# Optimization experiments

Measured on AMD Instinct MI355X. Metric: run time of the kernel, lower is better.

Reference implementation:

```python
import jax, jax.numpy as jnp
import numpy as np

B, S, V = 2, 336, 8      # batch, seq_len, n_vars
D, H, P = 256, 8, 96     # d_model, num_heads, pred_len
DK = D // H
OUT_CHN = 8
EPS = 1e-5


def _layernorm(x, g, b):
    mu = jnp.mean(x, axis=-1, keepdims=True)
    var = jnp.var(x, axis=-1, keepdims=True)
    return (x - mu) * jax.lax.rsqrt(var + EPS) * g + b


def _attn_ff(src, Wq, bq, Wk, bk, Wv, bv, Wo, bo, ln1_g, ln1_b):
    # src: [N, L, D]; manual MHA + residual + layernorm (dropout=0)
    N, L, _ = src.shape
    q = (src @ Wq + bq).reshape(N, L, H, DK).transpose(0, 2, 1, 3)
    k = (src @ Wk + bk).reshape(N, L, H, DK).transpose(0, 2, 1, 3)
    v = (src @ Wv + bv).reshape(N, L, H, DK).transpose(0, 2, 1, 3)
    scores = jnp.einsum('nhqd,nhkd->nhqk', q, k) / np.sqrt(DK).astype(np.float32)
    attn = jax.nn.softmax(scores, axis=-1)
    o = jnp.einsum('nhqk,nhkd->nhqd', attn, v)
    o = o.transpose(0, 2, 1, 3).reshape(N, L, D) @ Wo + bo
    return _layernorm(src + o, ln1_g, ln1_b)


def setup_inputs() -> dict:
    key = jax.random.key(0)
    ks = jax.random.split(key, 8)
    s = 1.0 / np.sqrt(D)
    return {
        'x': jax.random.normal(ks[0], (B, S, V), dtype=jnp.float32),
        'emb_w': jax.random.normal(ks[1], (1, D), dtype=jnp.float32),
        'emb_b': jnp.zeros((D,), jnp.float32),
        'Wq': jax.random.normal(ks[2], (D, D), dtype=jnp.float32) * s,
        'bq': jnp.zeros((D,), jnp.float32),
        'Wk': jax.random.normal(ks[3], (D, D), dtype=jnp.float32) * s,
        'bk': jnp.zeros((D,), jnp.float32),
        'Wv': jax.random.normal(ks[4], (D, D), dtype=jnp.float32) * s,
        'bv': jnp.zeros((D,), jnp.float32),
        'Wo': jax.random.normal(ks[5], (D, D), dtype=jnp.float32) * s,
        'bo': jnp.zeros((D,), jnp.float32),
        'ln1_g': jnp.ones((D,), jnp.float32),
        'ln1_b': jnp.zeros((D,), jnp.float32),
        'norm_g': jnp.ones((D,), jnp.float32),
        'norm_b': jnp.zeros((D,), jnp.float32),
        'proj_w': jax.random.normal(ks[6], (S * D, P), dtype=jnp.float32) / np.sqrt(S * D).astype(np.float32),
        'proj_b': jnp.zeros((P,), jnp.float32),
    }


def reference(x, emb_w, emb_b, Wq, bq, Wk, bk, Wv, bv, Wo, bo,
              ln1_g, ln1_b, norm_g, norm_b, proj_w, proj_b):
    attn_p = (Wq, bq, Wk, bk, Wv, bv, Wo, bo, ln1_g, ln1_b)
    # x: [B,S,V] -> [B,V,S] -> embed each scalar to D
    e = x.transpose(0, 2, 1)[..., None] @ emb_w + emb_b  # [B,V,S,D]
    for _ in range(10):
        # attention over time axis (shared weights)
        e = _attn_ff(e.reshape(B * V, S, D), *attn_p).reshape(B, V, S, D)
        e = _layernorm(e.transpose(0, 2, 1, 3), norm_g, norm_b)  # [B,S,V,D]
        # attention over variable axis (same weights)
        e = _attn_ff(e.reshape(B * S, V, D), *attn_p).reshape(B, S, V, D)
        e = e.transpose(0, 2, 1, 3)  # [B,V,S,D]
    out = e.reshape(B, V, S * D) @ proj_w + proj_b  # [B,V,P]
    return out.transpose(0, 2, 1)[:, :, :OUT_CHN]  # [B,P,out_chn]
```

## Files before the change

### kernel.cpp

```cpp
#include <hip/hip_runtime.h>

#define SS 336
#define VV 8
#define DD 256
#define DKK 32
#define NTOK 5376
#define NTD (NTOK * DD)
#define ATT_SCALE 0.17677669529663687f
#define LN_EPS 1e-5f

typedef _Float16 f16x8 __attribute__((ext_vector_type(8)));
typedef _Float16 f16x4v __attribute__((ext_vector_type(4)));
typedef __attribute__((ext_vector_type(4))) float f32x4;

__device__ inline _Float16 f2h(float f) { return (_Float16)f; }

__global__ __launch_bounds__(256) void k_prep_w(
    const float* __restrict__ Wq, const float* __restrict__ Wk,
    const float* __restrict__ Wv, const float* __restrict__ Wo,
    _Float16* __restrict__ WT2) {
  int z = blockIdx.y;
  const float* W = (z == 0) ? Wq : (z == 1) ? Wk : (z == 2) ? Wv : Wo;
  int o = blockIdx.x * 256 + threadIdx.x;
  int blk = o >> 9;
  int idx = o & 511;
  int lane = idx >> 3, j = idx & 7;
  int nt = blk >> 3, kb = blk & 7;
  int lcol = lane & 15, quad = lane >> 4;
  int n = nt * 16 + lcol;
  int k = kb * 32 + quad * 8 + j;
  WT2[(size_t)z * 65536 + o] = f2h(W[k * 256 + n]);
}

__global__ __launch_bounds__(256) void k_embed(
    const float* __restrict__ x, const float* __restrict__ ew,
    const float* __restrict__ eb, float* __restrict__ E,
    _Float16* __restrict__ E16) {
  int token = blockIdx.x;
  int n = token / SS, s = token - n * SS;
  int b = n >> 3, v = n & 7;
  float xv = x[(b * SS + s) * VV + v];
  int d = threadIdx.x;
  float val = fmaf(xv, ew[d], eb[d]);
  E[token * DD + d] = val;
  E16[token * DD + d] = f2h(val);
}

__global__ __launch_bounds__(256) void k_gemm_qkv(
    const _Float16* __restrict__ A16, const _Float16* __restrict__ WT2,
    const float* __restrict__ c0, const float* __restrict__ c1,
    const float* __restrict__ c2,
    _Float16* __restrict__ H0, _Float16* __restrict__ H1,
    _Float16* __restrict__ H2) {
  int z = blockIdx.z;
  const float* bias = (z == 0) ? c0 : (z == 1) ? c1 : c2;
  _Float16* H       = (z == 0) ? H0 : (z == 1) ? H1 : H2;
  int m0 = blockIdx.x * 64;
  int tid = threadIdx.x;
  int wave = tid >> 6, lane = tid & 63;
  int wm = wave >> 1, wn = wave & 1;
  int quad = lane >> 4, lcol = lane & 15;
  int ntb = blockIdx.y * 8 + wn * 4;

  __shared__ _Float16 As[64 * 264];

  for (int c = tid; c < 2048; c += 256) {
    int row = c >> 5, seg = c & 31;
    *(f16x8*)&As[row * 264 + seg * 8] =
        *(const f16x8*)&A16[(size_t)(m0 + row) * 256 + seg * 8];
  }
  __syncthreads();

  f32x4 acc[2][4] = {};

  for (int kb = 0; kb < 8; ++kb) {
    int k0 = kb * 32;
    f16x8 af[2];
#pragma unroll
    for (int mt = 0; mt < 2; ++mt)
      af[mt] = *(const f16x8*)&As[(wm * 32 + mt * 16 + lcol) * 264 + k0 + quad * 8];
#pragma unroll
    for (int nt = 0; nt < 4; ++nt) {
      f16x8 bfr = *(const f16x8*)&WT2[(size_t)z * 65536 +
                                      ((ntb + nt) * 8 + kb) * 512 + lane * 8];
#pragma unroll
      for (int mt = 0; mt < 2; ++mt)
        acc[mt][nt] = __builtin_amdgcn_mfma_f32_16x16x32_f16(
            af[mt], bfr, acc[mt][nt], 0, 0, 0);
    }
  }

  float bsv[4];
#pragma unroll
  for (int nt = 0; nt < 4; ++nt) bsv[nt] = bias[(ntb + nt) * 16 + lcol];
#pragma unroll
  for (int mt = 0; mt < 2; ++mt) {
#pragma unroll
    for (int i = 0; i < 4; ++i) {
      int r = m0 + wm * 32 + mt * 16 + quad * 4 + i;
#pragma unroll
      for (int nt = 0; nt < 4; ++nt) {
        int c = (ntb + nt) * 16 + lcol;
        H[(size_t)r * 256 + c] = f2h(acc[mt][nt][i] + bsv[nt]);
      }
    }
  }
}

#define KSTR 36
#define VTSTR 344
#define PSTR 72
__global__ __launch_bounds__(512) void k_attn_time(
    const _Float16* __restrict__ Q, const _Float16* __restrict__ K,
    const _Float16* __restrict__ V, _Float16* __restrict__ O16) {
  int qg = blockIdx.x, h = blockIdx.y, n = blockIdx.z;
  int tid = threadIdx.x;
  int wave = tid >> 6, lane = tid & 63;
  int quad = lane >> 4, lcol = lane & 15;

  __shared__ _Float16 Ks[336 * KSTR];
  __shared__ _Float16 Vt[32 * VTSTR + 16];
  __shared__ _Float16 Ps[8][16 * PSTR];

  const size_t base = (size_t)(n * SS) * DD + h * DKK;

  for (int c = tid; c < 1344; c += 512) {
    int row = c >> 2, part = c & 3;
    f16x8 kv = *(const f16x8*)&K[base + (size_t)row * DD + part * 8];
    f16x4v klo = __builtin_shufflevector(kv, kv, 0, 1, 2, 3);
    f16x4v khi = __builtin_shufflevector(kv, kv, 4, 5, 6, 7);
    *(f16x4v*)&Ks[row * KSTR + part * 8] = klo;
    *(f16x4v*)&Ks[row * KSTR + part * 8 + 4] = khi;
    f16x8 vv = *(const f16x8*)&V[base + (size_t)row * DD + part * 8];
#pragma unroll
    for (int j = 0; j < 8; ++j) Vt[(part * 8 + j) * VTSTR + row] = vv[j];
  }
  for (int c = tid; c < 272; c += 512) {
    if (c < 256) {
      int d = c >> 3, col = 336 + (c & 7);
      Vt[d * VTSTR + col] = (_Float16)0.f;
    } else {
      Vt[32 * VTSTR + (c - 256)] = (_Float16)0.f;
    }
  }
  __syncthreads();

  _Float16* P = Ps[wave];
  const f16x8 onesv = {(_Float16)1.f, (_Float16)1.f, (_Float16)1.f, (_Float16)1.f,
                       (_Float16)1.f, (_Float16)1.f, (_Float16)1.f, (_Float16)1.f};
  const f32x4 z4 = {0.f, 0.f, 0.f, 0.f};

  int qt0 = qg ? 11 : 0;
  int qtend = qg ? 21 : 11;
  for (int qtile = qt0 + wave; qtile < qtend; qtile += 8) {
    int qb = qtile * 16;

    f16x8 qf = *(const f16x8*)&Q[base + (size_t)(qb + lcol) * DD + quad * 8];
    f32x4 accA = {0.f, 0.f, 0.f, 0.f};
    f32x4 accB = {0.f, 0.f, 0.f, 0.f};
    f32x4 lacc = {0.f, 0.f, 0.f, 0.f};
    float m_[4] = {-1e30f, -1e30f, -1e30f, -1e30f};

    for (int T = 0; T < 6; ++T) {
      int k0 = T * 64;
      bool full = (T < 5);
      f32x4 s[4];
      {
        const _Float16* kp = &Ks[(k0 + lcol) * KSTR + quad * 8];
        f16x4v a0 = *(const f16x4v*)kp;
        f16x4v b0 = *(const f16x4v*)(kp + 4);
        f16x8 kf = __builtin_shufflevector(a0, b0, 0, 1, 2, 3, 4, 5, 6, 7);
        s[0] = __builtin_amdgcn_mfma_f32_16x16x32_f16(qf, kf, z4, 0, 0, 0);
      }
      if (full) {
#pragma unroll
        for (int u = 1; u < 4; ++u) {
          const _Float16* kp = &Ks[(k0 + u * 16 + lcol) * KSTR + quad * 8];
          f16x4v a0 = *(const f16x4v*)kp;
          f16x4v b0 = *(const f16x4v*)(kp + 4);
          f16x8 kf = __builtin_shufflevector(a0, b0, 0, 1, 2, 3, 4, 5, 6, 7);
          s[u] = __builtin_amdgcn_mfma_f32_16x16x32_f16(qf, kf, z4, 0, 0, 0);
        }
      } else {
        s[1] = z4; s[2] = z4; s[3] = z4;
      }
      float sc[4][4], p[4][4], corr[4];
#pragma unroll
      for (int u = 0; u < 4; ++u)
#pragma unroll
        for (int i = 0; i < 4; ++i)
          sc[u][i] = (u == 0 || full) ? s[u][i] * ATT_SCALE : -1e30f;
#pragma unroll
      for (int i = 0; i < 4; ++i) {
        float t2 = fmaxf(fmaxf(sc[0][i], sc[1][i]), fmaxf(sc[2][i], sc[3][i]));
        t2 = fmaxf(t2, __shfl_xor(t2, 1));
        t2 = fmaxf(t2, __shfl_xor(t2, 2));
        t2 = fmaxf(t2, __shfl_xor(t2, 4));
        t2 = fmaxf(t2, __shfl_xor(t2, 8));
        float nm = fmaxf(m_[i], t2);
        corr[i] = __expf(m_[i] - nm);
        m_[i] = nm;
#pragma unroll
        for (int u = 0; u < 4; ++u) p[u][i] = __expf(sc[u][i] - nm);
        accA[i] *= corr[i];
        accB[i] *= corr[i];
        lacc[i] *= corr[i];
      }
#pragma unroll
      for (int i = 0; i < 4; ++i)
#pragma unroll
        for (int u = 0; u < 4; ++u)
          P[(quad * 4 + i) * PSTR + u * 16 + lcol] = f2h(p[u][i]);
      f16x8 pf0 = *(const f16x8*)&P[lcol * PSTR + quad * 8];
      lacc = __builtin_amdgcn_mfma_f32_16x16x32_f16(pf0, onesv, lacc, 0, 0, 0);
      f16x8 va0 = *(const f16x8*)&Vt[lcol * VTSTR + k0 + quad * 8];
      f16x8 vb0 = *(const f16x8*)&Vt[(16 + lcol) * VTSTR + k0 + quad * 8];
      accA = __builtin_amdgcn_mfma_f32_16x16x32_f16(pf0, va0, accA, 0, 0, 0);
      accB = __builtin_amdgcn_mfma_f32_16x16x32_f16(pf0, vb0, accB, 0, 0, 0);
      if (full) {
        f16x8 pf1 = *(const f16x8*)&P[lcol * PSTR + 32 + quad * 8];
        lacc = __builtin_amdgcn_mfma_f32_16x16x32_f16(pf1, onesv, lacc, 0, 0, 0);
        f16x8 va1 = *(const f16x8*)&Vt[lcol * VTSTR + k0 + 32 + quad * 8];
        f16x8 vb1 = *(const f16x8*)&Vt[(16 + lcol) * VTSTR + k0 + 32 + quad * 8];
        accA = __builtin_amdgcn_mfma_f32_16x16x32_f16(pf1, va1, accA, 0, 0, 0);
        accB = __builtin_amdgcn_mfma_f32_16x16x32_f16(pf1, vb1, accB, 0, 0, 0);
      }
    }

#pragma unroll
    for (int i = 0; i < 4; ++i) {
      float inv = 1.f / lacc[i];
      P[(quad * 4 + i) * PSTR + lcol] = f2h(accA[i] * inv);
      P[(quad * 4 + i) * PSTR + 16 + lcol] = f2h(accB[i] * inv);
    }
    int row = lane >> 2, seg = lane & 3;
    f16x8 ov = *(const f16x8*)&P[row * PSTR + seg * 8];
    *(f16x8*)&O16[base + (size_t)(qb + row) * DD + seg * 8] = ov;
  }
}

__global__ __launch_bounds__(512) void k_mega_var(
    const _Float16* __restrict__ AO16, const _Float16* __restrict__ WT2,
    const float* __restrict__ bq, const float* __restrict__ bk,
    const float* __restrict__ bv, const float* __restrict__ bo,
    const float* __restrict__ g1, const float* __restrict__ c1,
    const float* __restrict__ gn, const float* __restrict__ bn,
    float* __restrict__ Etime, _Float16* __restrict__ Q16,
    _Float16* __restrict__ K16, _Float16* __restrict__ V16, int doqkv) {
  int tid = threadIdx.x;
  int wave = tid >> 6, lane = tid & 63;
  int quad = lane >> 4, lcol = lane & 15;

  __shared__ int rmapS[32];
  __shared__ _Float16 Af[32 * 264];
  __shared__ float Cf[32 * 260];
  __shared__ _Float16 QKVs[32 * 776];

  if (tid < 32) {
    int r2 = blockIdx.x * 32 + tid;
    int n_idx = r2 >> 3, v = r2 & 7;
    int b = n_idx / SS, s = n_idx - b * SS;
    rmapS[tid] = (b * VV + v) * SS + s;
  }
  __syncthreads();

  {
    int row = tid >> 4, seg = tid & 15;
    const _Float16* src = AO16 + (size_t)rmapS[row] * DD + seg * 16;
    _Float16* dst = Af + row * 264 + seg * 16;
    *(f16x8*)(dst) = *(const f16x8*)(src);
    *(f16x8*)(dst + 8) = *(const f16x8*)(src + 8);
  }
  __syncthreads();

  const _Float16* WoF = WT2 + (size_t)3 * 65536;

  {
    f32x4 acc[2][2] = {};
    for (int kb = 0; kb < 8; ++kb) {
      int k0 = kb * 32;
      f16x8 af0 = *(const f16x8*)&Af[lcol * 264 + k0 + quad * 8];
      f16x8 af1 = *(const f16x8*)&Af[(16 + lcol) * 264 + k0 + quad * 8];
#pragma unroll
      for (int nt = 0; nt < 2; ++nt) {
        f16x8 bfr = *(const f16x8*)&WoF[((wave * 2 + nt) * 8 + kb) * 512 + lane * 8];
        acc[0][nt] = __builtin_amdgcn_mfma_f32_16x16x32_f16(af0, bfr, acc[0][nt], 0, 0, 0);
        acc[1][nt] = __builtin_amdgcn_mfma_f32_16x16x32_f16(af1, bfr, acc[1][nt], 0, 0, 0);
      }
    }
#pragma unroll
    for (int mt = 0; mt < 2; ++mt) {
#pragma unroll
      for (int i = 0; i < 4; ++i) {
        int row = mt * 16 + quad * 4 + i;
        size_t rb = (size_t)rmapS[row] * 256;
#pragma unroll
        for (int nt = 0; nt < 2; ++nt) {
          int col = (wave * 2 + nt) * 16 + lcol;
          Cf[row * 260 + col] = acc[mt][nt][i] + bo[col] + Etime[rb + col];
        }
      }
    }
  }
  __syncthreads();

  {
    int row = tid >> 4, c0 = (tid & 15) * 16;
    float v[16];
#pragma unroll
    for (int j = 0; j < 16; ++j) v[j] = Cf[row * 260 + c0 + j];
#pragma unroll
    for (int pass = 0; pass < 2; ++pass) {
      const float* gg = pass ? gn : g1;
      const float* bb = pass ? bn : c1;
      float s = 0.f, q = 0.f;
#pragma unroll
      for (int j = 0; j < 16; ++j) { s += v[j]; q = fmaf(v[j], v[j], q); }
      s += __shfl_xor(s, 1); q += __shfl_xor(q, 1);
      s += __shfl_xor(s, 2); q += __shfl_xor(q, 2);
      s += __shfl_xor(s, 4); q += __shfl_xor(q, 4);
      s += __shfl_xor(s, 8); q += __shfl_xor(q, 8);
      float mu = s * (1.0f / 256.0f);
      float rs = rsqrtf(q * (1.0f / 256.0f) - mu * mu + LN_EPS);
#pragma unroll
      for (int j = 0; j < 16; ++j)
        v[j] = fmaf((v[j] - mu) * rs, gg[c0 + j], bb[c0 + j]);
    }
#pragma unroll
    for (int j = 0; j < 16; ++j) Cf[row * 260 + c0 + j] = v[j];
#pragma unroll
    for (int j8 = 0; j8 < 2; ++j8) {
      f16x8 h;
#pragma unroll
      for (int jj = 0; jj < 8; ++jj) h[jj] = f2h(v[j8 * 8 + jj]);
      *(f16x8*)&Af[row * 264 + c0 + j8 * 8] = h;
    }
  }
  __syncthreads();

  {
    f32x4 acc[2][6] = {};
    for (int kb = 0; kb < 8; ++kb) {
      int k0 = kb * 32;
      f16x8 af0 = *(const f16x8*)&Af[lcol * 264 + k0 + quad * 8];
      f16x8 af1 = *(const f16x8*)&Af[(16 + lcol) * 264 + k0 + quad * 8];
#pragma unroll
      for (int j = 0; j < 6; ++j) {
        int ntg = wave * 6 + j;
        f16x8 bfr = *(const f16x8*)&WT2[(size_t)(ntg * 8 + kb) * 512 + lane * 8];
        acc[0][j] = __builtin_amdgcn_mfma_f32_16x16x32_f16(af0, bfr, acc[0][j], 0, 0, 0);
        acc[1][j] = __builtin_amdgcn_mfma_f32_16x16x32_f16(af1, bfr, acc[1][j], 0, 0, 0);
      }
    }
#pragma unroll
    for (int j = 0; j < 6; ++j) {
      int ntg = wave * 6 + j;
      int colb = ntg * 16;
      int z = colb >> 8, coln = (colb & 255) + lcol;
      const float* bz = (z == 0) ? bq : (z == 1) ? bk : bv;
      float bval = bz[coln];
#pragma unroll
      for (int mt = 0; mt < 2; ++mt) {
#pragma unroll
        for (int i = 0; i < 4; ++i)
          QKVs[(mt * 16 + quad * 4 + i) * 776 + colb + lcol] = f2h(acc[mt][j][i] + bval);
      }
    }
  }
  __syncthreads();

  {
    int half = tid & 1, qi = (tid >> 1) & 7, h = (tid >> 4) & 7, ng = tid >> 7;
    int d0 = h * 32 + half * 16;
    const _Float16* Qp = &QKVs[(ng * 8 + qi) * 776 + d0];
    float qv[16];
#pragma unroll
    for (int j8 = 0; j8 < 2; ++j8) {
      f16x8 t = *(const f16x8*)(Qp + j8 * 8);
#pragma unroll
      for (int jj = 0; jj < 8; ++jj) qv[j8 * 8 + jj] = (float)t[jj];
    }
    float sc[8];
#pragma unroll
    for (int k = 0; k < 8; ++k) {
      const _Float16* Kp = &QKVs[(ng * 8 + k) * 776 + 256 + d0];
      float s = 0.f;
#pragma unroll
      for (int j8 = 0; j8 < 2; ++j8) {
        f16x8 t = *(const f16x8*)(Kp + j8 * 8);
#pragma unroll
        for (int jj = 0; jj < 8; ++jj) s = fmaf(qv[j8 * 8 + jj], (float)t[jj], s);
      }
      sc[k] = s;
    }
#pragma unroll
    for (int k = 0; k < 8; ++k)
      sc[k] = (sc[k] + __shfl_xor(sc[k], 1)) * ATT_SCALE;
    float mx = sc[0];
#pragma unroll
    for (int k = 1; k < 8; ++k) mx = fmaxf(mx, sc[k]);
    float ps = 0.f;
#pragma unroll
    for (int k = 0; k < 8; ++k) { sc[k] = __expf(sc[k] - mx); ps += sc[k]; }
    float inv = 1.f / ps;
    float ov[16];
#pragma unroll
    for (int j = 0; j < 16; ++j) ov[j] = 0.f;
#pragma unroll
    for (int k = 0; k < 8; ++k) {
      const _Float16* Vp = &QKVs[(ng * 8 + k) * 776 + 512 + d0];
      float p = sc[k];
#pragma unroll
      for (int j8 = 0; j8 < 2; ++j8) {
        f16x8 t = *(const f16x8*)(Vp + j8 * 8);
#pragma unroll
        for (int jj = 0; jj < 8; ++jj)
          ov[j8 * 8 + jj] = fmaf(p, (float)t[jj], ov[j8 * 8 + jj]);
      }
    }
    _Float16* Op = &Af[(ng * 8 + qi) * 264 + d0];
#pragma unroll
    for (int j8 = 0; j8 < 2; ++j8) {
      f16x8 hh;
#pragma unroll
      for (int jj = 0; jj < 8; ++jj) hh[jj] = f2h(ov[j8 * 8 + jj] * inv);
      *(f16x8*)(Op + j8 * 8) = hh;
    }
  }
  __syncthreads();

  {
    f32x4 acc[2][2] = {};
    for (int kb = 0; kb < 8; ++kb) {
      int k0 = kb * 32;
      f16x8 af0 = *(const f16x8*)&Af[lcol * 264 + k0 + quad * 8];
      f16x8 af1 = *(const f16x8*)&Af[(16 + lcol) * 264 + k0 + quad * 8];
#pragma unroll
      for (int nt = 0; nt < 2; ++nt) {
        f16x8 bfr = *(const f16x8*)&WoF[((wave * 2 + nt) * 8 + kb) * 512 + lane * 8];
        acc[0][nt] = __builtin_amdgcn_mfma_f32_16x16x32_f16(af0, bfr, acc[0][nt], 0, 0, 0);
        acc[1][nt] = __builtin_amdgcn_mfma_f32_16x16x32_f16(af1, bfr, acc[1][nt], 0, 0, 0);
      }
    }
#pragma unroll
    for (int mt = 0; mt < 2; ++mt) {
#pragma unroll
      for (int i = 0; i < 4; ++i) {
        int row = mt * 16 + quad * 4 + i;
#pragma unroll
        for (int nt = 0; nt < 2; ++nt) {
          int col = (wave * 2 + nt) * 16 + lcol;
          Cf[row * 260 + col] = acc[mt][nt][i] + bo[col] + Cf[row * 260 + col];
        }
      }
    }
  }
  __syncthreads();

  {
    int row = tid >> 4, c0 = (tid & 15) * 16;
    float v[16];
#pragma unroll
    for (int j = 0; j < 16; ++j) v[j] = Cf[row * 260 + c0 + j];
    float s = 0.f, q = 0.f;
#pragma unroll
    for (int j = 0; j < 16; ++j) { s += v[j]; q = fmaf(v[j], v[j], q); }
    s += __shfl_xor(s, 1); q += __shfl_xor(q, 1);
    s += __shfl_xor(s, 2); q += __shfl_xor(q, 2);
    s += __shfl_xor(s, 4); q += __shfl_xor(q, 4);
    s += __shfl_xor(s, 8); q += __shfl_xor(q, 8);
    float mu = s * (1.0f / 256.0f);
    float rs = rsqrtf(q * (1.0f / 256.0f) - mu * mu + LN_EPS);
#pragma unroll
    for (int j = 0; j < 16; ++j)
      v[j] = fmaf((v[j] - mu) * rs, g1[c0 + j], c1[c0 + j]);
    size_t rb = (size_t)rmapS[row] * 256 + c0;
#pragma unroll
    for (int j4 = 0; j4 < 4; ++j4) {
      float4 f4 = make_float4(v[j4 * 4], v[j4 * 4 + 1], v[j4 * 4 + 2], v[j4 * 4 + 3]);
      *(float4*)&Etime[rb + j4 * 4] = f4;
    }
#pragma unroll
    for (int j8 = 0; j8 < 2; ++j8) {
      f16x8 hh;
#pragma unroll
      for (int jj = 0; jj < 8; ++jj) hh[jj] = f2h(v[j8 * 8 + jj]);
      *(f16x8*)&Af[row * 264 + c0 + j8 * 8] = hh;
    }
  }
  __syncthreads();

  if (doqkv) {
    f32x4 acc[2][6] = {};
    for (int kb = 0; kb < 8; ++kb) {
      int k0 = kb * 32;
      f16x8 af0 = *(const f16x8*)&Af[lcol * 264 + k0 + quad * 8];
      f16x8 af1 = *(const f16x8*)&Af[(16 + lcol) * 264 + k0 + quad * 8];
#pragma unroll
      for (int j = 0; j < 6; ++j) {
        int ntg = wave * 6 + j;
        f16x8 bfr = *(const f16x8*)&WT2[(size_t)(ntg * 8 + kb) * 512 + lane * 8];
        acc[0][j] = __builtin_amdgcn_mfma_f32_16x16x32_f16(af0, bfr, acc[0][j], 0, 0, 0);
        acc[1][j] = __builtin_amdgcn_mfma_f32_16x16x32_f16(af1, bfr, acc[1][j], 0, 0, 0);
      }
    }
#pragma unroll
    for (int j = 0; j < 6; ++j) {
      int ntg = wave * 6 + j;
      int colb = ntg * 16;
      int z = colb >> 8, coln = (colb & 255) + lcol;
      const float* bz = (z == 0) ? bq : (z == 1) ? bk : bv;
      _Float16* Hd = (z == 0) ? Q16 : (z == 1) ? K16 : V16;
      float bval = bz[coln];
#pragma unroll
      for (int mt = 0; mt < 2; ++mt) {
#pragma unroll
        for (int i = 0; i < 4; ++i) {
          int row = mt * 16 + quad * 4 + i;
          Hd[(size_t)rmapS[row] * 256 + coln] = f2h(acc[mt][j][i] + bval);
        }
      }
    }
  }
}

__global__ __launch_bounds__(192) void k_proj_partial(
    const float* __restrict__ E, const float* __restrict__ PW,
    float* __restrict__ Part) {
  int kc = blockIdx.x;
  int tid = threadIdx.x;
  int p4 = tid % 24, g = tid / 24;
  __shared__ float Es[16][128];
  __shared__ float sm[8][1536];
  for (int idx = tid; idx < 512; idx += 192) {
    int row = idx >> 5, kk4 = idx & 31;
    *(float4*)&Es[row][kk4 * 4] =
        *(const float4*)&E[(size_t)row * 86016 + kc * 128 + kk4 * 4];
  }
  __syncthreads();
  float4 acc[16];
#pragma unroll
  for (int i = 0; i < 16; ++i) acc[i] = make_float4(0.f, 0.f, 0.f, 0.f);
  for (int j = 0; j < 16; ++j) {
    int k = g * 16 + j;
    float4 w = *(const float4*)&PW[(size_t)(kc * 128 + k) * 96 + p4 * 4];
#pragma unroll
    for (int row = 0; row < 16; ++row) {
      float e = Es[row][k];
      acc[row].x = fmaf(e, w.x, acc[row].x);
      acc[row].y = fmaf(e, w.y, acc[row].y);
      acc[row].z = fmaf(e, w.z, acc[row].z);
      acc[row].w = fmaf(e, w.w, acc[row].w);
    }
  }
#pragma unroll
  for (int row = 0; row < 16; ++row)
    *(float4*)&sm[g][row * 96 + p4 * 4] = acc[row];
  __syncthreads();
  for (int o = tid; o < 1536; o += 192) {
    float s = 0.f;
#pragma unroll
    for (int g2 = 0; g2 < 8; ++g2) s += sm[g2][o];
    Part[(size_t)kc * 1536 + o] = s;
  }
}

__global__ __launch_bounds__(256) void k_proj_reduce(
    const float* __restrict__ Part, const float* __restrict__ PB,
    float* __restrict__ out) {
  __shared__ float red[4][16];
  int tid = threadIdx.x;
  int j = (blockIdx.x << 4) | (tid & 15);
  int cg = tid >> 4;
  float s = 0.f;
#pragma unroll 7
  for (int i = 0; i < 42; ++i) {
    int c = cg * 42 + i;
    s += Part[(size_t)c * 1536 + j];
  }
  s += __shfl_xor(s, 16);
  s += __shfl_xor(s, 32);
  int wv = tid >> 6;
  if ((tid & 63) < 16) red[wv][tid & 15] = s;
  __syncthreads();
  if (tid < 16) {
    float t = red[0][tid] + red[1][tid] + red[2][tid] + red[3][tid];
    int jj = (blockIdx.x << 4) | tid;
    int row = jj / 96, p = jj - row * 96;
    int b = row >> 3, v = row & 7;
    out[b * 768 + p * 8 + v] = PB[p] + t;
  }
}

extern "C" void kernel_launch(void* const* d_in, const int* in_sizes, int n_in,
                              void* d_out, int out_size, void* d_ws,
                              size_t ws_size, hipStream_t stream) {
  const float* x     = (const float*)d_in[0];
  const float* emb_w = (const float*)d_in[1];
  const float* emb_b = (const float*)d_in[2];
  const float* Wq = (const float*)d_in[3];
  const float* bq = (const float*)d_in[4];
  const float* Wk = (const float*)d_in[5];
  const float* bk = (const float*)d_in[6];
  const float* Wv = (const float*)d_in[7];
  const float* bv = (const float*)d_in[8];
  const float* Wo = (const float*)d_in[9];
  const float* bo = (const float*)d_in[10];
  const float* g1 = (const float*)d_in[11];
  const float* b1 = (const float*)d_in[12];
  const float* gn = (const float*)d_in[13];
  const float* bn = (const float*)d_in[14];
  const float* PW = (const float*)d_in[15];
  const float* PB = (const float*)d_in[16];
  float* out = (float*)d_out;

  float* ws = (float*)d_ws;
  float* Etime   = ws;
  _Float16* Et16 = (_Float16*)(ws + (size_t)NTD);
  _Float16* Q16  = (_Float16*)(ws + (size_t)NTD + NTD / 2);
  _Float16* K16  = Q16 + (size_t)NTD;
  _Float16* V16  = K16 + (size_t)NTD;
  _Float16* AO16 = V16 + (size_t)NTD;
  _Float16* WT2  = AO16 + (size_t)NTD;
  float* Part    = (float*)(WT2 + 4 * 65536);

  k_prep_w<<<dim3(256, 4), 256, 0, stream>>>(Wq, Wk, Wv, Wo, WT2);
  k_embed<<<NTOK, 256, 0, stream>>>(x, emb_w, emb_b, Etime, Et16);
  k_gemm_qkv<<<dim3(84, 2, 3), 256, 0, stream>>>(
      Et16, WT2, bq, bk, bv, Q16, K16, V16);
  for (int it = 0; it < 10; ++it) {
    k_attn_time<<<dim3(2, 8, 16), 512, 0, stream>>>(Q16, K16, V16, AO16);
    k_mega_var<<<168, 512, 0, stream>>>(
        AO16, WT2, bq, bk, bv, bo, g1, b1, gn, bn, Etime,
        Q16, K16, V16, (it < 9) ? 1 : 0);
  }
  k_proj_partial<<<672, 192, 0, stream>>>(Etime, PW, Part);
  k_proj_reduce<<<96, 256, 0, stream>>>(Part, PB, out);
}
```

Before: 571.8 us.

## Fuse QKV projection into time-attention kernel, drop separate QKV GEMM

Moves the Q/K/V projection for the time-axis attention into the attention kernel itself. Each block loads its head's weight slices into LDS and computes K, V (full sequence) and Q (its query tiles) directly into shared memory. The mega_var kernel now writes only the fp16 normalized activations instead of Q/K/V, which removes the QKV global round-trip and the standalone QKV GEMM launch. The cost is that K/V projections are recomputed by both query-group blocks per head. The attention kernel also uses about 143KB of LDS, which limits occupancy to one block per CU.

```diff
diff --git a/kernel.cpp b/kernel.cpp
--- a/kernel.cpp
+++ b/kernel.cpp
@@ -46,116 +46,105 @@
   E16[token * DD + d] = f2h(val);
 }
 
-__global__ __launch_bounds__(256) void k_gemm_qkv(
-    const _Float16* __restrict__ A16, const _Float16* __restrict__ WT2,
-    const float* __restrict__ c0, const float* __restrict__ c1,
-    const float* __restrict__ c2,
-    _Float16* __restrict__ H0, _Float16* __restrict__ H1,
-    _Float16* __restrict__ H2) {
-  int z = blockIdx.z;
-  const float* bias = (z == 0) ? c0 : (z == 1) ? c1 : c2;
-  _Float16* H       = (z == 0) ? H0 : (z == 1) ? H1 : H2;
-  int m0 = blockIdx.x * 64;
-  int tid = threadIdx.x;
-  int wave = tid >> 6, lane = tid & 63;
-  int wm = wave >> 1, wn = wave & 1;
-  int quad = lane >> 4, lcol = lane & 15;
-  int ntb = blockIdx.y * 8 + wn * 4;
-
-  __shared__ _Float16 As[64 * 264];
-
-  for (int c = tid; c < 2048; c += 256) {
-    int row = c >> 5, seg = c & 31;
-    *(f16x8*)&As[row * 264 + seg * 8] =
-        *(const f16x8*)&A16[(size_t)(m0 + row) * 256 + seg * 8];
-  }
-  __syncthreads();
-
-  f32x4 acc[2][4] = {};
-
-  for (int kb = 0; kb < 8; ++kb) {
-    int k0 = kb * 32;
-    f16x8 af[2];
-#pragma unroll
-    for (int mt = 0; mt < 2; ++mt)
-      af[mt] = *(const f16x8*)&As[(wm * 32 + mt * 16 + lcol) * 264 + k0 + quad * 8];
-#pragma unroll
-    for (int nt = 0; nt < 4; ++nt) {
-      f16x8 bfr = *(const f16x8*)&WT2[(size_t)z * 65536 +
-                                      ((ntb + nt) * 8 + kb) * 512 + lane * 8];
-#pragma unroll
-      for (int mt = 0; mt < 2; ++mt)
-        acc[mt][nt] = __builtin_amdgcn_mfma_f32_16x16x32_f16(
-            af[mt], bfr, acc[mt][nt], 0, 0, 0);
-    }
-  }
-
-  float bsv[4];
-#pragma unroll
-  for (int nt = 0; nt < 4; ++nt) bsv[nt] = bias[(ntb + nt) * 16 + lcol];
-#pragma unroll
-  for (int mt = 0; mt < 2; ++mt) {
-#pragma unroll
-    for (int i = 0; i < 4; ++i) {
-      int r = m0 + wm * 32 + mt * 16 + quad * 4 + i;
-#pragma unroll
-      for (int nt = 0; nt < 4; ++nt) {
-        int c = (ntb + nt) * 16 + lcol;
-        H[(size_t)r * 256 + c] = f2h(acc[mt][nt][i] + bsv[nt]);
-      }
-    }
-  }
-}
-
 #define KSTR 36
 #define VTSTR 344
 #define PSTR 72
+#define QSTR 40
 __global__ __launch_bounds__(512) void k_attn_time(
-    const _Float16* __restrict__ Q, const _Float16* __restrict__ K,
-    const _Float16* __restrict__ V, _Float16* __restrict__ O16) {
+    const _Float16* __restrict__ Et16, const _Float16* __restrict__ WT2,
+    const float* __restrict__ bq, const float* __restrict__ bk,
+    const float* __restrict__ bv, _Float16* __restrict__ O16) {
   int qg = blockIdx.x, h = blockIdx.y, n = blockIdx.z;
   int tid = threadIdx.x;
   int wave = tid >> 6, lane = tid & 63;
   int quad = lane >> 4, lcol = lane & 15;
 
-  __shared__ _Float16 Ks[336 * KSTR];
-  __shared__ _Float16 Vt[32 * VTSTR + 16];
-  __shared__ _Float16 Ps[8][16 * PSTR];
-
-  const size_t base = (size_t)(n * SS) * DD + h * DKK;
-
-  for (int c = tid; c < 1344; c += 512) {
-    int row = c >> 2, part = c & 3;
-    f16x8 kv = *(const f16x8*)&K[base + (size_t)row * DD + part * 8];
-    f16x4v klo = __builtin_shufflevector(kv, kv, 0, 1, 2, 3);
-    f16x4v khi = __builtin_shufflevector(kv, kv, 4, 5, 6, 7);
-    *(f16x4v*)&Ks[row * KSTR + part * 8] = klo;
-    *(f16x4v*)&Ks[row * KSTR + part * 8 + 4] = khi;
-    f16x8 vv = *(const f16x8*)&V[base + (size_t)row * DD + part * 8];
-#pragma unroll
-    for (int j = 0; j < 8; ++j) Vt[(part * 8 + j) * VTSTR + row] = vv[j];
-  }
-  for (int c = tid; c < 272; c += 512) {
-    if (c < 256) {
-      int d = c >> 3, col = 336 + (c & 7);
-      Vt[d * VTSTR + col] = (_Float16)0.f;
-    } else {
-      Vt[32 * VTSTR + (c - 256)] = (_Float16)0.f;
-    }
-  }
-  __syncthreads();
-
-  _Float16* P = Ps[wave];
+  __shared__ __align__(16) char SMRAW[143264];
+  _Float16* Ks  = (_Float16*)SMRAW;
+  _Float16* Vt  = (_Float16*)(SMRAW + 24192);
+  _Float16* Qs  = (_Float16*)(SMRAW + 46240);
+  _Float16* Wl  = (_Float16*)(SMRAW + 60320);
+  _Float16* Ach = (_Float16*)(SMRAW + 109472);
+  _Float16* PsB = (_Float16*)(SMRAW + 60320);
+
+  const size_t ebase = (size_t)(n * SS) * DD;
+  const size_t base  = ebase + h * DKK;
+  int qt0 = qg ? 11 : 0;
+  int qtend = qg ? 21 : 11;
+
+  const f32x4 z4 = {0.f, 0.f, 0.f, 0.f};
+
+  {
+    int h2 = h * 2;
+    for (int c = tid; c < 3072; c += 512) {
+      int ot = c >> 9, rest = c & 511;
+      int z = (ot < 2) ? 1 : (ot < 4) ? 2 : 0;
+      int nt = h2 + (ot & 1);
+      *(f16x8*)&Wl[(ot << 12) + rest * 8] =
+          *(const f16x8*)&WT2[(size_t)z * 65536 + nt * 4096 + rest * 8];
+    }
+    for (int c = tid; c < 272; c += 512) {
+      if (c < 256) {
+        int d = c >> 3, col = 336 + (c & 7);
+        Vt[d * VTSTR + col] = (_Float16)0.f;
+      } else {
+        Vt[32 * VTSTR + (c - 256)] = (_Float16)0.f;
+      }
+    }
+  }
+
+  for (int ck = 0; ck < 6; ++ck) {
+    int m0c = ck * 64;
+    int nmt = (ck < 5) ? 4 : 1;
+    __syncthreads();
+    for (int c = tid; c < nmt * 16 * 32; c += 512) {
+      int row = c >> 5, seg = c & 31;
+      *(f16x8*)&Ach[row * 264 + seg * 8] =
+          *(const f16x8*)&Et16[ebase + (size_t)(m0c + row) * 256 + seg * 8];
+    }
+    __syncthreads();
+    int nU = nmt * 6;
+    for (int u = wave; u < nU; u += 8) {
+      int mtl = u / 6, ot = u % 6;
+      int gt = ck * 4 + mtl;
+      if (ot >= 4 && (gt < qt0 || gt >= qtend)) continue;
+      f32x4 acc = z4;
+#pragma unroll
+      for (int kb = 0; kb < 8; ++kb) {
+        f16x8 af = *(const f16x8*)&Ach[(mtl * 16 + lcol) * 264 + kb * 32 + quad * 8];
+        f16x8 wf = *(const f16x8*)&Wl[(ot << 12) + kb * 512 + lane * 8];
+        acc = __builtin_amdgcn_mfma_f32_16x16x32_f16(af, wf, acc, 0, 0, 0);
+      }
+      int dlo = ((ot & 1) << 4) + lcol;
+      const float* bz = (ot < 2) ? bk : (ot < 4) ? bv : bq;
+      float bval = bz[h * 32 + dlo];
+      if (ot < 2) {
+#pragma unroll
+        for (int i = 0; i < 4; ++i)
+          Ks[(m0c + mtl * 16 + quad * 4 + i) * KSTR + dlo] = f2h(acc[i] + bval);
+      } else if (ot < 4) {
+#pragma unroll
+        for (int i = 0; i < 4; ++i)
+          Vt[dlo * VTSTR + (m0c + mtl * 16 + quad * 4 + i)] = f2h(acc[i] + bval);
+      } else {
+        int ql = gt - qt0;
+#pragma unroll
+        for (int i = 0; i < 4; ++i)
+          Qs[(ql * 16 + quad * 4 + i) * QSTR + dlo] = f2h(acc[i] + bval);
+      }
+    }
+  }
+  __syncthreads();
+
+  _Float16* P = PsB + wave * (16 * PSTR);
   const f16x8 onesv = {(_Float16)1.f, (_Float16)1.f, (_Float16)1.f, (_Float16)1.f,
                        (_Float16)1.f, (_Float16)1.f, (_Float16)1.f, (_Float16)1.f};
-  const f32x4 z4 = {0.f, 0.f, 0.f, 0.f};
-
-  int qt0 = qg ? 11 : 0;
-  int qtend = qg ? 21 : 11;
+
   for (int qtile = qt0 + wave; qtile < qtend; qtile += 8) {
     int qb = qtile * 16;
-
-    f16x8 qf = *(const f16x8*)&Q[base + (size_t)(qb + lcol) * DD + quad * 8];
+    int ql = qtile - qt0;
+
+    f16x8 qf = *(const f16x8*)&Qs[(ql * 16 + lcol) * QSTR + quad * 8];
     f32x4 accA = {0.f, 0.f, 0.f, 0.f};
     f32x4 accB = {0.f, 0.f, 0.f, 0.f};
     f32x4 lacc = {0.f, 0.f, 0.f, 0.f};
@@ -245,8 +234,7 @@
     const float* __restrict__ bv, const float* __restrict__ bo,
     const float* __restrict__ g1, const float* __restrict__ c1,
     const float* __restrict__ gn, const float* __restrict__ bn,
-    float* __restrict__ Etime, _Float16* __restrict__ Q16,
-    _Float16* __restrict__ K16, _Float16* __restrict__ V16, int doqkv) {
+    float* __restrict__ Etime, _Float16* __restrict__ Et16) {
   int tid = threadIdx.x;
   int wave = tid >> 6, lane = tid & 63;
   int quad = lane >> 4, lcol = lane & 15;
@@ -485,41 +473,7 @@
       f16x8 hh;
 #pragma unroll
       for (int jj = 0; jj < 8; ++jj) hh[jj] = f2h(v[j8 * 8 + jj]);
-      *(f16x8*)&Af[row * 264 + c0 + j8 * 8] = hh;
-    }
-  }
-  __syncthreads();
-
-  if (doqkv) {
-    f32x4 acc[2][6] = {};
-    for (int kb = 0; kb < 8; ++kb) {
-      int k0 = kb * 32;
-      f16x8 af0 = *(const f16x8*)&Af[lcol * 264 + k0 + quad * 8];
-      f16x8 af1 = *(const f16x8*)&Af[(16 + lcol) * 264 + k0 + quad * 8];
-#pragma unroll
-      for (int j = 0; j < 6; ++j) {
-        int ntg = wave * 6 + j;
-        f16x8 bfr = *(const f16x8*)&WT2[(size_t)(ntg * 8 + kb) * 512 + lane * 8];
-        acc[0][j] = __builtin_amdgcn_mfma_f32_16x16x32_f16(af0, bfr, acc[0][j], 0, 0, 0);
-        acc[1][j] = __builtin_amdgcn_mfma_f32_16x16x32_f16(af1, bfr, acc[1][j], 0, 0, 0);
-      }
-    }
-#pragma unroll
-    for (int j = 0; j < 6; ++j) {
-      int ntg = wave * 6 + j;
-      int colb = ntg * 16;
-      int z = colb >> 8, coln = (colb & 255) + lcol;
-      const float* bz = (z == 0) ? bq : (z == 1) ? bk : bv;
-      _Float16* Hd = (z == 0) ? Q16 : (z == 1) ? K16 : V16;
-      float bval = bz[coln];
-#pragma unroll
-      for (int mt = 0; mt < 2; ++mt) {
-#pragma unroll
-        for (int i = 0; i < 4; ++i) {
-          int row = mt * 16 + quad * 4 + i;
-          Hd[(size_t)rmapS[row] * 256 + coln] = f2h(acc[mt][j][i] + bval);
-        }
-      }
+      *(f16x8*)&Et16[rb + j8 * 8] = hh;
     }
   }
 }
@@ -617,22 +571,17 @@
   float* ws = (float*)d_ws;
   float* Etime   = ws;
   _Float16* Et16 = (_Float16*)(ws + (size_t)NTD);
-  _Float16* Q16  = (_Float16*)(ws + (size_t)NTD + NTD / 2);
-  _Float16* K16  = Q16 + (size_t)NTD;
-  _Float16* V16  = K16 + (size_t)NTD;
-  _Float16* AO16 = V16 + (size_t)NTD;
+  _Float16* AO16 = Et16 + (size_t)NTD;
   _Float16* WT2  = AO16 + (size_t)NTD;
   float* Part    = (float*)(WT2 + 4 * 65536);
 
   k_prep_w<<<dim3(256, 4), 256, 0, stream>>>(Wq, Wk, Wv, Wo, WT2);
   k_embed<<<NTOK, 256, 0, stream>>>(x, emb_w, emb_b, Etime, Et16);
-  k_gemm_qkv<<<dim3(84, 2, 3), 256, 0, stream>>>(
-      Et16, WT2, bq, bk, bv, Q16, K16, V16);
   for (int it = 0; it < 10; ++it) {
-    k_attn_time<<<dim3(2, 8, 16), 512, 0, stream>>>(Q16, K16, V16, AO16);
+    k_attn_time<<<dim3(2, 8, 16), 512, 0, stream>>>(
+        Et16, WT2, bq, bk, bv, AO16);
     k_mega_var<<<168, 512, 0, stream>>>(
-        AO16, WT2, bq, bk, bv, bo, g1, b1, gn, bn, Etime,
-        Q16, K16, V16, (it < 9) ? 1 : 0);
+        AO16, WT2, bq, bk, bv, bo, g1, b1, gn, bn, Etime, Et16);
   }
   k_proj_partial<<<672, 192, 0, stream>>>(Etime, PW, Part);
   k_proj_reduce<<<96, 256, 0, stream>>>(Part, PB, out);
```

Measured after the change: 587.7 us. 2.8% more time.
